# Kernel tuning notes

Hardware: AMD Instinct MI355X
Metric: run time of the kernel (lower is better)

The kernel has to match this reference:

```python
import jax, jax.numpy as jnp
import numpy as np

B, LQ, LK, D = 2, 2048, 2048, 1024
H, DK, DV = 16, 64, 64
EPS = 1e-6


def setup_inputs() -> dict:
    key = jax.random.key(0)
    ks = jax.random.split(key, 12)
    s = 1.0 / np.sqrt(D)
    return {
        "PE_states": jax.random.normal(ks[0], (B, LK, D), jnp.float32),
        "global_state": jax.random.normal(ks[1], (B, LQ, D), jnp.float32),
        "PE_statements": jax.random.normal(ks[2], (B, LK, D), jnp.float32),
        "PE_operators": jax.random.normal(ks[3], (B, LK, D), jnp.float32),
        "PE_solution_scores": jax.random.uniform(ks[4], (B, LK), jnp.float32),
        "mask": jax.random.randint(ks[5], (B, LQ, LK), 0, 2, jnp.int32),
        "w_q": jax.random.normal(ks[6], (D, H * DK), jnp.float32) * s,
        "w_k": jax.random.normal(ks[7], (D, H * DK), jnp.float32) * s,
        "w_v": jax.random.normal(ks[8], (D, H * DV), jnp.float32) * s,
        "w_fc": jax.random.normal(ks[9], (H * DV, D), jnp.float32) * s,
        "ln_gamma": jnp.ones((D,), jnp.float32),
        "ln_beta": jnp.zeros((D,), jnp.float32),
    }


def _layer_norm(x, gamma, beta):
    mu = jnp.mean(x, axis=-1, keepdims=True)
    var = jnp.mean(jnp.square(x - mu), axis=-1, keepdims=True)
    return (x - mu) * jax.lax.rsqrt(var + EPS) * gamma + beta


def reference(PE_states, global_state, PE_statements, PE_operators,
              PE_solution_scores, mask, w_q, w_k, w_v, w_fc, ln_gamma, ln_beta):
    # att_type == 'ca_sc', query_mode == 'PE', dropout == 0
    residual = global_state  # [B, LQ, D]
    q = (global_state @ w_q).reshape(B, LQ, H, DK).transpose(0, 2, 1, 3)   # bhqd
    k = (PE_states @ w_k).reshape(B, LK, H, DK).transpose(0, 2, 1, 3)      # bhkd
    v_s = (PE_statements @ w_v).reshape(B, LK, H, DV).transpose(0, 2, 1, 3)
    v_o = (PE_operators @ w_v).reshape(B, LK, H, DV).transpose(0, 2, 1, 3)

    temp = jnp.asarray(DK, jnp.float32) ** 0.5
    attn = jnp.einsum('bhqd,bhkd->bhqk', q / temp, k)  # [B,H,LQ,LK]
    # PE_solution_scores: per-key bias broadcast over heads and queries
    attn = (attn + PE_solution_scores[:, None, None, :]) / 2.0
    attn = jnp.where(mask[:, None, :, :] == 0, jnp.float32(-1e9), attn)
    attn = jax.nn.softmax(attn, axis=-1)

    def head_out(v):
        o = jnp.einsum('bhqk,bhkd->bhqd', attn, v)
        o = o.transpose(0, 2, 1, 3).reshape(B, LQ, H * DV)
        o = o @ w_fc + residual
        return _layer_norm(o, ln_gamma, ln_beta)

    statement_pred = head_out(v_s)
    operator_pred = head_out(v_o)
    return statement_pred, operator_pred
```

## Files before the change

### kernel.cpp

```cpp
#include <hip/hip_runtime.h>


typedef unsigned short u16;
typedef unsigned int   u32;
typedef unsigned long long u64;

typedef __attribute__((ext_vector_type(8))) short frag_ab;
typedef __attribute__((ext_vector_type(4))) float frag_cd;
typedef __attribute__((ext_vector_type(8))) unsigned short u16x8;
typedef __attribute__((ext_vector_type(4))) unsigned short u16x4;

__device__ __forceinline__ u16 f2bf(float f) {
    u32 x = __builtin_bit_cast(u32, f);
    return (u16)((x + 0x7fffu + ((x >> 16) & 1u)) >> 16);
}
__device__ __forceinline__ u16 f2bf_trunc(float f) {
    return (u16)(__builtin_bit_cast(u32, f) >> 16);
}

#define GLDS16(gsrc, ldst)                                                     \
    __builtin_amdgcn_global_load_lds(                                          \
        (const __attribute__((address_space(1))) void*)(gsrc),                 \
        (__attribute__((address_space(3))) void*)(ldst), 16, 0, 0)

__global__ __launch_bounds__(256) void downcast_kernel(
    const float* __restrict__ in0, const float* __restrict__ in1,
    const float* __restrict__ in2, const float* __restrict__ in3,
    u16* __restrict__ out)
{
    int z = blockIdx.y;
    const float* in = z == 0 ? in0 : z == 1 ? in1 : z == 2 ? in2 : in3;
    u16* o = out + (size_t)z * 4194304;
    size_t i = ((size_t)blockIdx.x * 256 + threadIdx.x) * 8;
    float4 f0 = *(const float4*)(in + i);
    float4 f1 = *(const float4*)(in + i + 4);
    u16x8 t;
    t[0] = f2bf(f0.x); t[1] = f2bf(f0.y); t[2] = f2bf(f0.z); t[3] = f2bf(f0.w);
    t[4] = f2bf(f1.x); t[5] = f2bf(f1.y); t[6] = f2bf(f1.z); t[7] = f2bf(f1.w);
    *(u16x8*)(o + i) = t;
}

__global__ __launch_bounds__(256) void transpose_kernel(
    const float* __restrict__ w_q, const float* __restrict__ w_k,
    const float* __restrict__ w_v, const float* __restrict__ w_fc,
    u16* __restrict__ wqT, u16* __restrict__ wkT,
    u16* __restrict__ wvT, u16* __restrict__ wfcT)
{
    __shared__ u16 tile[32][33];
    int z = blockIdx.z;
    const float* in = z == 0 ? w_q : z == 1 ? w_k : z == 2 ? w_v : w_fc;
    u16* out = z == 0 ? wqT : z == 1 ? wkT : z == 2 ? wvT : wfcT;
    int bx = blockIdx.x * 32, by = blockIdx.y * 32;
    int tx = threadIdx.x & 31, ty = threadIdx.x >> 5;
    for (int i = 0; i < 32; i += 8)
        tile[ty + i][tx] = f2bf(in[(size_t)(by + ty + i) * 1024 + bx + tx]);
    __syncthreads();
    for (int i = 0; i < 32; i += 8)
        out[(size_t)(bx + ty + i) * 1024 + by + tx] = tile[tx][ty + i];
}

__global__ __launch_bounds__(256) void pack_mask_kernel(
    const int* __restrict__ mask, u64* __restrict__ bits)
{
    long long gid = (long long)blockIdx.x * 256 + threadIdx.x;
    int v = mask[gid];
    u64 bl = __ballot(v != 0);
    if ((threadIdx.x & 63) == 0) bits[gid >> 6] = bl;
}

__device__ __forceinline__ void gemm_core(
    const u16* __restrict__ A, const u16* __restrict__ BT,
    int bm, int bn, u16* Al, u16* Bl, frag_cd acc[4][4])
{
    const int tid = threadIdx.x;
    const int wave = tid >> 6, lane = tid & 63;
    const int ln15 = lane & 15, quad = lane >> 4;
    const int wm4 = (wave & 1) * 4, wn4 = (wave >> 1) * 4;

    for (int k0 = 0; k0 < 1024; k0 += 64) {
        for (int s = 0; s < 4; s++) {
            int f = wave * 4 + s;
            int grp = f >> 1, ks = f & 1;
            size_t col = k0 + ks * 32 + quad * 8;
            GLDS16(&A[(size_t)(bm + grp * 16 + ln15) * 1024 + col], Al + f * 512);
            GLDS16(&BT[(size_t)(bn + grp * 16 + ln15) * 1024 + col], Bl + f * 512);
        }
        __syncthreads();
        for (int ks = 0; ks < 2; ks++) {
            frag_ab a[4], b[4];
            for (int i = 0; i < 4; i++)
                a[i] = *(const frag_ab*)(Al + ((wm4 + i) * 2 + ks) * 512 + lane * 8);
            for (int j = 0; j < 4; j++)
                b[j] = *(const frag_ab*)(Bl + ((wn4 + j) * 2 + ks) * 512 + lane * 8);
            for (int i = 0; i < 4; i++)
                for (int j = 0; j < 4; j++)
                    acc[i][j] = __builtin_amdgcn_mfma_f32_16x16x32_bf16(a[i], b[j], acc[i][j], 0, 0, 0);
        }
        __syncthreads();
    }
}

__global__ __launch_bounds__(256, 3) void proj_gemm_kernel(
    const u16* __restrict__ Ab4,
    const u16* __restrict__ wqT, const u16* __restrict__ wkT, const u16* __restrict__ wvT,
    u16* __restrict__ Qb, u16* __restrict__ Kb,
    u16* __restrict__ VsT_g, u16* __restrict__ VoT_g)
{
    __shared__ alignas(16) u16 Al[16 * 512];
    __shared__ alignas(16) u16 Bl[16 * 512];
    const int z = blockIdx.z;
    const u16* A = Ab4 + (size_t)z * 4194304;
    const u16* BT = z == 0 ? wqT : z == 1 ? wkT : wvT;
    const int bm = blockIdx.x * 128, bn = blockIdx.y * 128;
    frag_cd acc[4][4] = {};
    gemm_core(A, BT, bm, bn, Al, Bl, acc);

    const int lane = threadIdx.x & 63;
    const int wave = threadIdx.x >> 6;
    const int ln15 = lane & 15, quad = lane >> 4;
    const int wm = (wave & 1) * 64, wn = (wave >> 1) * 64;
    if (z < 2) {
        u16* C = z == 0 ? Qb : Kb;
        for (int i = 0; i < 4; i++) for (int j = 0; j < 4; j++) {
            int row0 = bm + wm + i * 16 + quad * 4;
            int col = bn + wn + j * 16 + ln15;
            for (int r = 0; r < 4; r++)
                C[(size_t)(row0 + r) * 1024 + col] = f2bf(acc[i][j][r]);
        }
    } else {
        u16* C = z == 2 ? VsT_g : VoT_g;
        for (int i = 0; i < 4; i++) for (int j = 0; j < 4; j++) {
            int row0 = bm + wm + i * 16 + quad * 4;
            int col = bn + wn + j * 16 + ln15;
            u16x4 t;
            for (int r = 0; r < 4; r++) t[r] = f2bf(acc[i][j][r]);
            *(u16x4*)&C[(size_t)col * 4096 + row0] = t;
        }
    }
}

__global__ __launch_bounds__(256, 3) void fc_gemm_kernel(
    const u16* __restrict__ Osb, const u16* __restrict__ Oob, const u16* __restrict__ wfcT,
    const float* __restrict__ resid, float* __restrict__ preLN)
{
    __shared__ alignas(16) u16 Al[16 * 512];
    __shared__ alignas(16) u16 Bl[16 * 512];
    const int z = blockIdx.z;
    const u16* A = z == 0 ? Osb : Oob;
    float* Cf = preLN + (size_t)z * 4194304;
    const int bm = blockIdx.x * 128, bn = blockIdx.y * 128;
    frag_cd acc[4][4] = {};
    gemm_core(A, wfcT, bm, bn, Al, Bl, acc);

    const int lane = threadIdx.x & 63;
    const int wave = threadIdx.x >> 6;
    const int ln15 = lane & 15, quad = lane >> 4;
    const int wm = (wave & 1) * 64, wn = (wave >> 1) * 64;
    for (int i = 0; i < 4; i++) for (int j = 0; j < 4; j++) {
        int row0 = bm + wm + i * 16 + quad * 4;
        int col = bn + wn + j * 16 + ln15;
        for (int r = 0; r < 4; r++) {
            size_t off = (size_t)(row0 + r) * 1024 + col;
            Cf[off] = acc[i][j][r] + resid[off];
        }
    }
}

__device__ __forceinline__ void flash_stage(
    const u16* __restrict__ Kp, const u16* __restrict__ VsT, const u16* __restrict__ VoT,
    int b, int h, int kt, int wave, int ln15, int quad, u16* buf)
{
    const int k0 = kt * 64;
    for (int s = 0; s < 6; s++) {
        int t = wave * 6 + s;
        int f = t & 7;
        int grp = f >> 1, ks = f & 1;
        const u16* g;
        if (t < 8)
            g = &Kp[(size_t)(b * 2048 + k0 + grp * 16 + ln15) * 1024 + h * 64 + ks * 32 + quad * 8];
        else if (t < 16)
            g = &VsT[(size_t)(h * 64 + grp * 16 + ln15) * 4096 + b * 2048 + k0 + ks * 32 + quad * 8];
        else
            g = &VoT[(size_t)(h * 64 + grp * 16 + ln15) * 4096 + b * 2048 + k0 + ks * 32 + quad * 8];
        GLDS16(g, buf + t * 512);
    }
}

__global__ __launch_bounds__(256, 2) void flash_kernel(
    const u16* __restrict__ Q, const u16* __restrict__ Kp,
    const u16* __restrict__ VsT_g, const u16* __restrict__ VoT_g,
    const float* __restrict__ scores, const u64* __restrict__ mbits,
    u16* __restrict__ Os, u16* __restrict__ Oo)
{
    __shared__ alignas(16) u16 KV[2][24 * 512];
    __shared__ alignas(16) u16 Psm[4][32][72];
    const int qt = blockIdx.x, h = blockIdx.y, b = blockIdx.z;
    const int tid = threadIdx.x;
    const int wave = tid >> 6, lane = tid & 63;
    const int ln15 = lane & 15, quad = lane >> 4;
    const int qbase = b * 2048 + qt * 128 + wave * 32;

    frag_ab aq[2][2];
    for (int g = 0; g < 2; g++) {
        const u16* qp = &Q[(size_t)(qbase + g * 16 + ln15) * 1024 + h * 64 + quad * 8];
        aq[g][0] = *(const frag_ab*)qp;
        aq[g][1] = *(const frag_ab*)(qp + 32);
    }

    frag_cd os_[2][4] = {}, oo_[2][4] = {};
    float l_i[2][4] = {};

    flash_stage(Kp, VsT_g, VoT_g, b, h, 0, wave, ln15, quad, KV[0]);

    for (int kt = 0; kt < 32; kt++) {
        const int p = kt & 1;
        __syncthreads();
        if (kt < 31)
            flash_stage(Kp, VsT_g, VoT_g, b, h, kt + 1, wave, ln15, quad, KV[p ^ 1]);

        const u16* bufp = KV[p];
        const int k0 = kt * 64;

        float sc[4];
        for (int nt = 0; nt < 4; nt++)
            sc[nt] = scores[b * 2048 + k0 + nt * 16 + ln15] * 0.5f;
        u64 bits[2][4];
        for (int g = 0; g < 2; g++)
            for (int r = 0; r < 4; r++)
                bits[g][r] = mbits[(size_t)(qbase + g * 16 + quad * 4 + r) * 32 + kt];

        frag_cd s0[4] = {}, s1[4] = {};
        for (int ks = 0; ks < 2; ks++)
            for (int nt = 0; nt < 4; nt++) {
                frag_ab bk = *(const frag_ab*)(bufp + (nt * 2 + ks) * 512 + lane * 8);
                s0[nt] = __builtin_amdgcn_mfma_f32_16x16x32_bf16(aq[0][ks], bk, s0[nt], 0, 0, 0);
                s1[nt] = __builtin_amdgcn_mfma_f32_16x16x32_bf16(aq[1][ks], bk, s1[nt], 0, 0, 0);
            }

        for (int nt = 0; nt < 4; nt++)
            for (int r = 0; r < 4; r++) {
                float e0 = __expf(s0[nt][r] * 0.0625f + sc[nt]);
                if (!((bits[0][r] >> (nt * 16 + ln15)) & 1ull)) e0 = 0.0f;
                l_i[0][r] += e0;
                Psm[wave][quad * 4 + r][nt * 16 + ln15] = f2bf_trunc(e0);
                float e1 = __expf(s1[nt][r] * 0.0625f + sc[nt]);
                if (!((bits[1][r] >> (nt * 16 + ln15)) & 1ull)) e1 = 0.0f;
                l_i[1][r] += e1;
                Psm[wave][16 + quad * 4 + r][nt * 16 + ln15] = f2bf_trunc(e1);
            }

        frag_ab ap[2][2];
        for (int g = 0; g < 2; g++) {
            ap[g][0] = *(const frag_ab*)&Psm[wave][g * 16 + ln15][quad * 8];
            ap[g][1] = *(const frag_ab*)&Psm[wave][g * 16 + ln15][32 + quad * 8];
        }
        for (int ks = 0; ks < 2; ks++)
            for (int nt = 0; nt < 4; nt++) {
                frag_ab bs = *(const frag_ab*)(bufp + (8 + nt * 2 + ks) * 512 + lane * 8);
                frag_ab bo = *(const frag_ab*)(bufp + (16 + nt * 2 + ks) * 512 + lane * 8);
                os_[0][nt] = __builtin_amdgcn_mfma_f32_16x16x32_bf16(ap[0][ks], bs, os_[0][nt], 0, 0, 0);
                os_[1][nt] = __builtin_amdgcn_mfma_f32_16x16x32_bf16(ap[1][ks], bs, os_[1][nt], 0, 0, 0);
                oo_[0][nt] = __builtin_amdgcn_mfma_f32_16x16x32_bf16(ap[0][ks], bo, oo_[0][nt], 0, 0, 0);
                oo_[1][nt] = __builtin_amdgcn_mfma_f32_16x16x32_bf16(ap[1][ks], bo, oo_[1][nt], 0, 0, 0);
            }
    }

    for (int g = 0; g < 2; g++)
        for (int r = 0; r < 4; r++) {
            float s = l_i[g][r];
            for (int off = 1; off < 16; off <<= 1)
                s += __shfl_xor(s, off, 64);
            float inv = 1.0f / fmaxf(s, 1e-30f);
            for (int nt = 0; nt < 4; nt++) {
                size_t off2 = (size_t)(qbase + g * 16 + quad * 4 + r) * 1024 + h * 64 + nt * 16 + ln15;
                Os[off2] = f2bf(os_[g][nt][r] * inv);
                Oo[off2] = f2bf(oo_[g][nt][r] * inv);
            }
        }
}

__global__ __launch_bounds__(256) void ln_kernel(
    const float* __restrict__ X, const float* __restrict__ gamma, const float* __restrict__ beta,
    float* __restrict__ out)
{
    __shared__ float red[4];
    int row = blockIdx.x;
    int tid = threadIdx.x;
    const float* x = X + (size_t)row * 1024;
    float v[4];
    float s = 0.f;
    for (int i = 0; i < 4; i++) { v[i] = x[tid + i * 256]; s += v[i]; }
    for (int off = 1; off < 64; off <<= 1) s += __shfl_xor(s, off, 64);
    int wv = tid >> 6, ln = tid & 63;
    if (ln == 0) red[wv] = s;
    __syncthreads();
    float mean = (red[0] + red[1] + red[2] + red[3]) * (1.0f / 1024.0f);
    float s2 = 0.f;
    for (int i = 0; i < 4; i++) { float d = v[i] - mean; s2 += d * d; }
    for (int off = 1; off < 64; off <<= 1) s2 += __shfl_xor(s2, off, 64);
    __syncthreads();
    if (ln == 0) red[wv] = s2;
    __syncthreads();
    float var = (red[0] + red[1] + red[2] + red[3]) * (1.0f / 1024.0f);
    float rstd = rsqrtf(var + 1e-6f);
    for (int i = 0; i < 4; i++) {
        int c = tid + i * 256;
        out[(size_t)row * 1024 + c] = (v[i] - mean) * rstd * gamma[c] + beta[c];
    }
}

extern "C" void kernel_launch(void* const* d_in, const int* in_sizes, int n_in,
                              void* d_out, int out_size, void* d_ws, size_t ws_size,
                              hipStream_t stream)
{
    const float* PE_states     = (const float*)d_in[0];
    const float* global_state  = (const float*)d_in[1];
    const float* PE_statements = (const float*)d_in[2];
    const float* PE_operators  = (const float*)d_in[3];
    const float* scores        = (const float*)d_in[4];
    const int*   mask          = (const int*)d_in[5];
    const float* w_q  = (const float*)d_in[6];
    const float* w_k  = (const float*)d_in[7];
    const float* w_v  = (const float*)d_in[8];
    const float* w_fc = (const float*)d_in[9];
    const float* gamma = (const float*)d_in[10];
    const float* beta  = (const float*)d_in[11];
    float* out = (float*)d_out;

    char* ws = (char*)d_ws;
    const size_t MB = 1u << 20;
    u16* Ab4   = (u16*)(ws + 0 * MB);
    u16* Osb   = (u16*)(ws + 0 * MB);
    u16* Oob   = (u16*)(ws + 8 * MB);
    u16* wqT   = (u16*)(ws + 32 * MB);
    u16* wkT   = (u16*)(ws + 34 * MB);
    u16* wvT   = (u16*)(ws + 36 * MB);
    u16* wfcT  = (u16*)(ws + 38 * MB);
    u64* mbits = (u64*)(ws + 40 * MB);
    u16* Qb    = (u16*)(ws + 41 * MB);
    u16* Kb    = (u16*)(ws + 49 * MB);
    u16* VsT_g = (u16*)(ws + 57 * MB);
    u16* VoT_g = (u16*)(ws + 65 * MB);
    float* preLN = (float*)(ws + 41 * MB);

    downcast_kernel<<<dim3(2048, 4), 256, 0, stream>>>(
        global_state, PE_states, PE_statements, PE_operators, Ab4);
    transpose_kernel<<<dim3(32, 32, 4), 256, 0, stream>>>(w_q, w_k, w_v, w_fc, wqT, wkT, wvT, wfcT);
    pack_mask_kernel<<<32768, 256, 0, stream>>>(mask, mbits);

    proj_gemm_kernel<<<dim3(32, 8, 4), 256, 0, stream>>>(
        Ab4, wqT, wkT, wvT, Qb, Kb, VsT_g, VoT_g);

    flash_kernel<<<dim3(16, 16, 2), 256, 0, stream>>>(Qb, Kb, VsT_g, VoT_g, scores, mbits, Osb, Oob);

    fc_gemm_kernel<<<dim3(32, 8, 2), 256, 0, stream>>>(Osb, Oob, wfcT, global_state, preLN);
    ln_kernel<<<8192, 256, 0, stream>>>(preLN, gamma, beta, out);
}
```

Before: 395.1 us.

## Rewrite flash attention with 32x32 MFMA, transposed scores, and register-only P

Rewrites the attention inner loop around 32x32x16 bf16 MFMAs. S is computed transposed as K·Q, so each lane owns one query row and the probability tile can be repacked into A fragments with permlane32_swap instead of a round trip through shared memory. The scale 0.5/sqrt(dk)·log2e is folded into Q at projection time. The per-key score bias is injected through an extra MFMA using a split bf16 hi/lo pair against a ones vector, exp uses exp2, and masking is a bitwise AND. This removes the Psm LDS traffic and per-element scaling arithmetic, at the cost of bias precision from the bf16 split and more complex lane/row index mapping.

```diff
diff --git a/kernel.cpp b/kernel.cpp
--- a/kernel.cpp
+++ b/kernel.cpp
@@ -7,21 +7,28 @@
 
 typedef __attribute__((ext_vector_type(8))) short frag_ab;
 typedef __attribute__((ext_vector_type(4))) float frag_cd;
+typedef __attribute__((ext_vector_type(16))) float f32x16;
 typedef __attribute__((ext_vector_type(8))) unsigned short u16x8;
 typedef __attribute__((ext_vector_type(4))) unsigned short u16x4;
+typedef __attribute__((ext_vector_type(2))) unsigned int u32x2;
+typedef __attribute__((ext_vector_type(4))) int int4v;
 
 __device__ __forceinline__ u16 f2bf(float f) {
     u32 x = __builtin_bit_cast(u32, f);
     return (u16)((x + 0x7fffu + ((x >> 16) & 1u)) >> 16);
 }
-__device__ __forceinline__ u16 f2bf_trunc(float f) {
-    return (u16)(__builtin_bit_cast(u32, f) >> 16);
+
+__device__ __forceinline__ u32 pkbf(float a, float b) {
+    return __builtin_amdgcn_perm(__builtin_bit_cast(u32, b),
+                                 __builtin_bit_cast(u32, a), 0x07060302u);
 }
 
 #define GLDS16(gsrc, ldst)                                                     \
     __builtin_amdgcn_global_load_lds(                                          \
         (const __attribute__((address_space(1))) void*)(gsrc),                 \
         (__attribute__((address_space(3))) void*)(ldst), 16, 0, 0)
+
+#define MFMA32(a, b, c) __builtin_amdgcn_mfma_f32_32x32x16_bf16(a, b, c, 0, 0, 0)
 
 __global__ __launch_bounds__(256) void downcast_kernel(
     const float* __restrict__ in0, const float* __restrict__ in1,
@@ -121,11 +128,12 @@
     const int wm = (wave & 1) * 64, wn = (wave >> 1) * 64;
     if (z < 2) {
         u16* C = z == 0 ? Qb : Kb;
+        const float qsc = z == 0 ? 0.09016844f : 1.0f;
         for (int i = 0; i < 4; i++) for (int j = 0; j < 4; j++) {
             int row0 = bm + wm + i * 16 + quad * 4;
             int col = bn + wn + j * 16 + ln15;
             for (int r = 0; r < 4; r++)
-                C[(size_t)(row0 + r) * 1024 + col] = f2bf(acc[i][j][r]);
+                C[(size_t)(row0 + r) * 1024 + col] = f2bf(acc[i][j][r] * qsc);
         }
     } else {
         u16* C = z == 2 ? VsT_g : VoT_g;
@@ -168,20 +176,22 @@
 
 __device__ __forceinline__ void flash_stage(
     const u16* __restrict__ Kp, const u16* __restrict__ VsT, const u16* __restrict__ VoT,
-    int b, int h, int kt, int wave, int ln15, int quad, u16* buf)
+    int b, int h, int kt, int wave, int ln31, int hi, u16* buf)
 {
     const int k0 = kt * 64;
     for (int s = 0; s < 6; s++) {
         int t = wave * 6 + s;
-        int f = t & 7;
-        int grp = f >> 1, ks = f & 1;
         const u16* g;
-        if (t < 8)
-            g = &Kp[(size_t)(b * 2048 + k0 + grp * 16 + ln15) * 1024 + h * 64 + ks * 32 + quad * 8];
-        else if (t < 16)
-            g = &VsT[(size_t)(h * 64 + grp * 16 + ln15) * 4096 + b * 2048 + k0 + ks * 32 + quad * 8];
-        else
-            g = &VoT[(size_t)(h * 64 + grp * 16 + ln15) * 4096 + b * 2048 + k0 + ks * 32 + quad * 8];
+        if (t < 8) {
+            int n = t >> 2, ks = t & 3;
+            g = &Kp[(size_t)(b * 2048 + k0 + n * 32 + ln31) * 1024 + h * 64 + ks * 16 + hi * 8];
+        } else if (t < 16) {
+            int dt = (t >> 2) & 1, sk = t & 3;
+            g = &VsT[(size_t)(h * 64 + dt * 32 + ln31) * 4096 + b * 2048 + k0 + sk * 16 + hi * 8];
+        } else {
+            int dt = (t >> 2) & 1, sk = t & 3;
+            g = &VoT[(size_t)(h * 64 + dt * 32 + ln31) * 4096 + b * 2048 + k0 + sk * 16 + hi * 8];
+        }
         GLDS16(g, buf + t * 512);
     }
 }
@@ -193,90 +203,120 @@
     u16* __restrict__ Os, u16* __restrict__ Oo)
 {
     __shared__ alignas(16) u16 KV[2][24 * 512];
-    __shared__ alignas(16) u16 Psm[4][32][72];
     const int qt = blockIdx.x, h = blockIdx.y, b = blockIdx.z;
     const int tid = threadIdx.x;
     const int wave = tid >> 6, lane = tid & 63;
-    const int ln15 = lane & 15, quad = lane >> 4;
+    const int ln31 = lane & 31, hi = lane >> 5;
     const int qbase = b * 2048 + qt * 128 + wave * 32;
-
-    frag_ab aq[2][2];
-    for (int g = 0; g < 2; g++) {
-        const u16* qp = &Q[(size_t)(qbase + g * 16 + ln15) * 1024 + h * 64 + quad * 8];
-        aq[g][0] = *(const frag_ab*)qp;
-        aq[g][1] = *(const frag_ab*)(qp + 32);
-    }
-
-    frag_cd os_[2][4] = {}, oo_[2][4] = {};
-    float l_i[2][4] = {};
-
-    flash_stage(Kp, VsT_g, VoT_g, b, h, 0, wave, ln15, quad, KV[0]);
+    const int qrow = qbase + ln31;
+
+    frag_ab aq0, aq1, aq2, aq3;
+    {
+        const u16* qp = &Q[(size_t)qrow * 1024 + h * 64 + hi * 8];
+        aq0 = *(const frag_ab*)(qp);
+        aq1 = *(const frag_ab*)(qp + 16);
+        aq2 = *(const frag_ab*)(qp + 32);
+        aq3 = *(const frag_ab*)(qp + 48);
+    }
+    frag_ab bbias = {};
+    bbias[0] = (short)0x3F80; bbias[1] = (short)0x3F80;
+
+    f32x16 os0 = {}, os1 = {}, oo0 = {}, oo1 = {};
+    float l0 = 0.f, l1 = 0.f;
+    const int shl4 = 4 - 4 * hi;
+
+    auto softmax16 = [&](f32x16& s, u32 wa, float& lacc) {
+#pragma unroll
+        for (int r = 0; r < 16; r++) {
+            const int bitc = (r & 3) + 8 * (r >> 2);
+            u32 m = (u32)(((int)(wa << (27 - bitc))) >> 31);
+            float e = __builtin_amdgcn_exp2f(s[r]);
+            u32 pb = __builtin_bit_cast(u32, e) & m;
+            float pf = __builtin_bit_cast(float, pb);
+            lacc += pf;
+            s[r] = pf;
+        }
+    };
+
+    flash_stage(Kp, VsT_g, VoT_g, b, h, 0, wave, ln31, hi, KV[0]);
 
     for (int kt = 0; kt < 32; kt++) {
         const int p = kt & 1;
+        float sc0f = scores[b * 2048 + kt * 64 + ln31];
+        float sc1f = scores[b * 2048 + kt * 64 + 32 + ln31];
+        u64 w = mbits[(size_t)qrow * 32 + kt];
         __syncthreads();
         if (kt < 31)
-            flash_stage(Kp, VsT_g, VoT_g, b, h, kt + 1, wave, ln15, quad, KV[p ^ 1]);
-
+            flash_stage(Kp, VsT_g, VoT_g, b, h, kt + 1, wave, ln31, hi, KV[p ^ 1]);
         const u16* bufp = KV[p];
-        const int k0 = kt * 64;
-
-        float sc[4];
-        for (int nt = 0; nt < 4; nt++)
-            sc[nt] = scores[b * 2048 + k0 + nt * 16 + ln15] * 0.5f;
-        u64 bits[2][4];
-        for (int g = 0; g < 2; g++)
-            for (int r = 0; r < 4; r++)
-                bits[g][r] = mbits[(size_t)(qbase + g * 16 + quad * 4 + r) * 32 + kt];
-
-        frag_cd s0[4] = {}, s1[4] = {};
-        for (int ks = 0; ks < 2; ks++)
-            for (int nt = 0; nt < 4; nt++) {
-                frag_ab bk = *(const frag_ab*)(bufp + (nt * 2 + ks) * 512 + lane * 8);
-                s0[nt] = __builtin_amdgcn_mfma_f32_16x16x32_bf16(aq[0][ks], bk, s0[nt], 0, 0, 0);
-                s1[nt] = __builtin_amdgcn_mfma_f32_16x16x32_bf16(aq[1][ks], bk, s1[nt], 0, 0, 0);
-            }
-
-        for (int nt = 0; nt < 4; nt++)
-            for (int r = 0; r < 4; r++) {
-                float e0 = __expf(s0[nt][r] * 0.0625f + sc[nt]);
-                if (!((bits[0][r] >> (nt * 16 + ln15)) & 1ull)) e0 = 0.0f;
-                l_i[0][r] += e0;
-                Psm[wave][quad * 4 + r][nt * 16 + ln15] = f2bf_trunc(e0);
-                float e1 = __expf(s1[nt][r] * 0.0625f + sc[nt]);
-                if (!((bits[1][r] >> (nt * 16 + ln15)) & 1ull)) e1 = 0.0f;
-                l_i[1][r] += e1;
-                Psm[wave][16 + quad * 4 + r][nt * 16 + ln15] = f2bf_trunc(e1);
-            }
-
-        frag_ab ap[2][2];
-        for (int g = 0; g < 2; g++) {
-            ap[g][0] = *(const frag_ab*)&Psm[wave][g * 16 + ln15][quad * 8];
-            ap[g][1] = *(const frag_ab*)&Psm[wave][g * 16 + ln15][32 + quad * 8];
-        }
-        for (int ks = 0; ks < 2; ks++)
-            for (int nt = 0; nt < 4; nt++) {
-                frag_ab bs = *(const frag_ab*)(bufp + (8 + nt * 2 + ks) * 512 + lane * 8);
-                frag_ab bo = *(const frag_ab*)(bufp + (16 + nt * 2 + ks) * 512 + lane * 8);
-                os_[0][nt] = __builtin_amdgcn_mfma_f32_16x16x32_bf16(ap[0][ks], bs, os_[0][nt], 0, 0, 0);
-                os_[1][nt] = __builtin_amdgcn_mfma_f32_16x16x32_bf16(ap[1][ks], bs, os_[1][nt], 0, 0, 0);
-                oo_[0][nt] = __builtin_amdgcn_mfma_f32_16x16x32_bf16(ap[0][ks], bo, oo_[0][nt], 0, 0, 0);
-                oo_[1][nt] = __builtin_amdgcn_mfma_f32_16x16x32_bf16(ap[1][ks], bo, oo_[1][nt], 0, 0, 0);
-            }
-    }
-
-    for (int g = 0; g < 2; g++)
-        for (int r = 0; r < 4; r++) {
-            float s = l_i[g][r];
-            for (int off = 1; off < 16; off <<= 1)
-                s += __shfl_xor(s, off, 64);
-            float inv = 1.0f / fmaxf(s, 1e-30f);
-            for (int nt = 0; nt < 4; nt++) {
-                size_t off2 = (size_t)(qbase + g * 16 + quad * 4 + r) * 1024 + h * 64 + nt * 16 + ln15;
-                Os[off2] = f2bf(os_[g][nt][r] * inv);
-                Oo[off2] = f2bf(oo_[g][nt][r] * inv);
-            }
-        }
+
+        frag_ab ab0 = {}, ab1 = {};
+        if (!hi) {
+            float t0 = sc0f * 0.72134752f;
+            u16 c0 = f2bf(t0);
+            ab0[0] = (short)c0;
+            ab0[1] = (short)f2bf(t0 - __builtin_bit_cast(float, (u32)c0 << 16));
+            float t1 = sc1f * 0.72134752f;
+            u16 c1 = f2bf(t1);
+            ab1[0] = (short)c1;
+            ab1[1] = (short)f2bf(t1 - __builtin_bit_cast(float, (u32)c1 << 16));
+        }
+
+        f32x16 sacc0 = {}, sacc1 = {};
+        sacc0 = MFMA32(ab0, bbias, sacc0);
+        sacc1 = MFMA32(ab1, bbias, sacc1);
+#pragma unroll
+        for (int ks = 0; ks < 4; ks++) {
+            frag_ab ak0 = *(const frag_ab*)(bufp + (0 * 4 + ks) * 512 + lane * 8);
+            frag_ab ak1 = *(const frag_ab*)(bufp + (1 * 4 + ks) * 512 + lane * 8);
+            frag_ab q = ks == 0 ? aq0 : ks == 1 ? aq1 : ks == 2 ? aq2 : aq3;
+            sacc0 = MFMA32(ak0, q, sacc0);
+            sacc1 = MFMA32(ak1, q, sacc1);
+        }
+
+        u32 wa0 = ((u32)w) << shl4;
+        u32 wa1 = ((u32)(w >> 32)) << shl4;
+        softmax16(sacc0, wa0, l0);
+        softmax16(sacc1, wa1, l1);
+
+#pragma unroll
+        for (int sk = 0; sk < 4; sk++) {
+            const f32x16& ps = (sk < 2) ? sacc0 : sacc1;
+            const int e0 = (sk & 1) * 8;
+            u32 a0 = pkbf(ps[e0 + 0], ps[e0 + 1]);
+            u32 a1 = pkbf(ps[e0 + 2], ps[e0 + 3]);
+            u32 b0 = pkbf(ps[e0 + 4], ps[e0 + 5]);
+            u32 b1 = pkbf(ps[e0 + 6], ps[e0 + 7]);
+            u32x2 r0 = __builtin_amdgcn_permlane32_swap(a0, b0, false, false);
+            u32x2 r1 = __builtin_amdgcn_permlane32_swap(a1, b1, false, false);
+            int4v iv;
+            iv[0] = (int)r0[0]; iv[1] = (int)r1[0];
+            iv[2] = (int)r0[1]; iv[3] = (int)r1[1];
+            frag_ab ap = __builtin_bit_cast(frag_ab, iv);
+            frag_ab bs0 = *(const frag_ab*)(bufp + (8 + sk) * 512 + lane * 8);
+            frag_ab bs1 = *(const frag_ab*)(bufp + (12 + sk) * 512 + lane * 8);
+            frag_ab bo0 = *(const frag_ab*)(bufp + (16 + sk) * 512 + lane * 8);
+            frag_ab bo1 = *(const frag_ab*)(bufp + (20 + sk) * 512 + lane * 8);
+            os0 = MFMA32(ap, bs0, os0);
+            os1 = MFMA32(ap, bs1, os1);
+            oo0 = MFMA32(ap, bo0, oo0);
+            oo1 = MFMA32(ap, bo1, oo1);
+        }
+    }
+
+    float l_run = l0 + l1;
+    float l_tot = l_run + __shfl_xor(l_run, 32, 64);
+#pragma unroll
+    for (int r = 0; r < 16; r++) {
+        const int qr = (r & 3) + 8 * (r >> 2) + 4 * hi;
+        float lv = __shfl(l_tot, qr, 64);
+        float inv = 1.0f / fmaxf(lv, 1e-30f);
+        size_t row = (size_t)(qbase + qr) * 1024 + h * 64;
+        Os[row + ln31]      = f2bf(os0[r] * inv);
+        Os[row + 32 + ln31] = f2bf(os1[r] * inv);
+        Oo[row + ln31]      = f2bf(oo0[r] * inv);
+        Oo[row + 32 + ln31] = f2bf(oo1[r] * inv);
+    }
 }
 
 __global__ __launch_bounds__(256) void ln_kernel(
```

New measurement: 373.3 us. 1.06x faster.
